# Performance work log

Hardware: AMD Instinct MI355X
Metric: run time of the kernel (lower is better)

The kernel has to match this reference:

```python
import jax, jax.numpy as jnp
import numpy as np

BIAS = (1, 1)


def setup_inputs() -> dict:
    key = jax.random.key(0)
    k1, k2 = jax.random.split(key)
    B, N = 32, 1024
    c = jax.random.normal(k1, (B, 2 * N), dtype=jnp.float32)
    y = jax.random.randint(k2, (B, N), 0, 2, dtype=jnp.int32)
    return {"c": c, "y": y}


def reference(c, y):
    # split_tensor: even columns -> c1 (scores c_{2r}), odd columns -> s1 (thresholds s_{2r+1})
    c1 = c[:, ::2]   # [B, N]
    s1 = c[:, 1::2]  # [B, N]
    yf = y.astype(jnp.float32)
    y_bar = 1.0 - yf

    y_norm = jnp.sum(yf, axis=1) ** BIAS[0]
    y_bar_norm = jnp.sum(y_bar, axis=1) ** BIAS[1]
    denom = 2.0 * y_norm * y_bar_norm + y_norm * y_norm + y_bar_norm * y_bar_norm

    # pairwise_sub_exp(a, b, x) = sum_{k,l} a_k b_l exp(x_l - x_k)
    #                           = (sum_k a_k e^{-x_k}) * (sum_l b_l e^{x_l})  -- fused, no [B,N,N] materialization
    y_exp_neg_c1 = jnp.sum(yf * jnp.exp(-c1), axis=1)      # sum_k y_k e^{-c1_k}
    ybar_exp_c1 = jnp.sum(y_bar * jnp.exp(c1), axis=1)     # sum_l ybar_l e^{c1_l}
    ybar_exp_neg_s1 = jnp.sum(y_bar * jnp.exp(-s1), axis=1)
    y_exp_s1 = jnp.sum(yf * jnp.exp(s1), axis=1)

    p1 = y_exp_neg_c1 * ybar_exp_c1        # pairwise_sub_exp(y, y_bar, c1)
    p2 = ybar_exp_neg_s1 * y_exp_s1        # pairwise_sub_exp(y_bar, y, s1)
    # valueThreshod_sub_exp(a, x, s) = sum_{r,t} a_r a_t exp(s_t - x_r)
    v1 = y_exp_neg_c1 * y_exp_s1           # valueThreshod_sub_exp(y, c1, s1)
    v2 = ybar_exp_neg_s1 * ybar_exp_c1     # valueThreshod_sub_exp(y_bar, s1, c1)

    return jnp.mean((p1 + p2 + v1 + v2) / denom)
```

## Files before the change

### kernel.cpp

```cpp
#include <hip/hip_runtime.h>

#define NCOLS 1024
#define NROWS 32

__global__ __launch_bounds__(256) void bpmll_row_kernel(
    const float* __restrict__ c, const int* __restrict__ y,
    float* __restrict__ ws) {
    const int row = blockIdx.x;
    const int tid = threadIdx.x;
    const float2* __restrict__ crow =
        reinterpret_cast<const float2*>(c + (size_t)row * 2 * NCOLS);
    const int* __restrict__ yrow = y + (size_t)row * NCOLS;

    float sy = 0.f, sA = 0.f, sB = 0.f, sC = 0.f, sD = 0.f;
    #pragma unroll
    for (int k = 0; k < NCOLS / 256; ++k) {
        const int col = k * 256 + tid;
        const float2 cs = crow[col];
        const float yf = (float)yrow[col];
        const float yb = 1.f - yf;
        const float ec  = __expf(cs.x);
        const float enc = __expf(-cs.x);
        const float es  = __expf(cs.y);
        const float ens = __expf(-cs.y);
        sy += yf;
        sA += yf * enc;
        sC += yb * ec;
        sB += yb * ens;
        sD += yf * es;
    }
    #pragma unroll
    for (int off = 32; off > 0; off >>= 1) {
        sy += __shfl_down(sy, off);
        sA += __shfl_down(sA, off);
        sB += __shfl_down(sB, off);
        sC += __shfl_down(sC, off);
        sD += __shfl_down(sD, off);
    }
    __shared__ float red[4][5];
    const int wave = tid >> 6;
    const int lane = tid & 63;
    if (lane == 0) {
        red[wave][0] = sy; red[wave][1] = sA; red[wave][2] = sB;
        red[wave][3] = sC; red[wave][4] = sD;
    }
    __syncthreads();
    if (tid == 0) {
        float ty = 0.f, tA = 0.f, tB = 0.f, tC = 0.f, tD = 0.f;
        #pragma unroll
        for (int w = 0; w < 4; ++w) {
            ty += red[w][0]; tA += red[w][1]; tB += red[w][2];
            tC += red[w][3]; tD += red[w][4];
        }
        const float yn  = ty;
        const float ybn = (float)NCOLS - ty;
        const float denom = 2.f * yn * ybn + yn * yn + ybn * ybn;
        ws[row] = (tA + tB) * (tC + tD) / denom;
    }
}

__global__ __launch_bounds__(64) void bpmll_final_kernel(
    const float* __restrict__ ws, float* __restrict__ out) {
    const int lane = threadIdx.x;
    float v = (lane < NROWS) ? ws[lane] : 0.f;
    #pragma unroll
    for (int off = 32; off > 0; off >>= 1) v += __shfl_down(v, off);
    if (lane == 0) out[0] = v * (1.f / NROWS);
}

extern "C" void kernel_launch(void* const* d_in, const int* in_sizes, int n_in,
                              void* d_out, int out_size, void* d_ws, size_t ws_size,
                              hipStream_t stream) {
    const float* c = (const float*)d_in[0];
    const int*   y = (const int*)d_in[1];
    float* out = (float*)d_out;
    float* ws  = (float*)d_ws;
    bpmll_row_kernel<<<NROWS, 256, 0, stream>>>(c, y, ws);
    bpmll_final_kernel<<<1, 64, 0, stream>>>(ws, out);
}
```

Before: 11.29 us.

## Fuse row and final reductions into one single-block kernel with fewer exps

```diff
diff --git a/kernel.cpp b/kernel.cpp
--- a/kernel.cpp
+++ b/kernel.cpp
@@ -3,69 +3,71 @@
 #define NCOLS 1024
 #define NROWS 32
 
-__global__ __launch_bounds__(256) void bpmll_row_kernel(
+__global__ __launch_bounds__(1024) void bpmll_fused_kernel(
     const float* __restrict__ c, const int* __restrict__ y,
-    float* __restrict__ ws) {
-    const int row = blockIdx.x;
+    float* __restrict__ out) {
     const int tid = threadIdx.x;
-    const float2* __restrict__ crow =
-        reinterpret_cast<const float2*>(c + (size_t)row * 2 * NCOLS);
-    const int* __restrict__ yrow = y + (size_t)row * NCOLS;
-
-    float sy = 0.f, sA = 0.f, sB = 0.f, sC = 0.f, sD = 0.f;
-    #pragma unroll
-    for (int k = 0; k < NCOLS / 256; ++k) {
-        const int col = k * 256 + tid;
-        const float2 cs = crow[col];
-        const float yf = (float)yrow[col];
-        const float yb = 1.f - yf;
-        const float ec  = __expf(cs.x);
-        const float enc = __expf(-cs.x);
-        const float es  = __expf(cs.y);
-        const float ens = __expf(-cs.y);
-        sy += yf;
-        sA += yf * enc;
-        sC += yb * ec;
-        sB += yb * ens;
-        sD += yf * es;
-    }
-    #pragma unroll
-    for (int off = 32; off > 0; off >>= 1) {
-        sy += __shfl_down(sy, off);
-        sA += __shfl_down(sA, off);
-        sB += __shfl_down(sB, off);
-        sC += __shfl_down(sC, off);
-        sD += __shfl_down(sD, off);
-    }
-    __shared__ float red[4][5];
     const int wave = tid >> 6;
     const int lane = tid & 63;
-    if (lane == 0) {
-        red[wave][0] = sy; red[wave][1] = sA; red[wave][2] = sB;
-        red[wave][3] = sC; red[wave][4] = sD;
+    __shared__ float rowv[NROWS];
+
+    #pragma unroll
+    for (int rr = 0; rr < 2; ++rr) {
+        const int row = wave * 2 + rr;
+        const float4* __restrict__ crow4 =
+            reinterpret_cast<const float4*>(c + (size_t)row * 2 * NCOLS);
+        const int2* __restrict__ yrow2 =
+            reinterpret_cast<const int2*>(y + (size_t)row * NCOLS);
+
+        float sy = 0.f, sA = 0.f, sB = 0.f, sC = 0.f, sD = 0.f;
+        #pragma unroll
+        for (int k = 0; k < 8; ++k) {
+            const int idx = k * 64 + lane;
+            const float4 F = crow4[idx];
+            const int2  Y = yrow2[idx];
+            {
+                const bool yy = (Y.x != 0);
+                const float e1 = __expf(yy ? -F.x : F.x);
+                const float e2 = __expf(yy ?  F.y : -F.y);
+                sy += yy ? 1.f : 0.f;
+                sA += yy ? e1 : 0.f;
+                sD += yy ? e2 : 0.f;
+                sC += yy ? 0.f : e1;
+                sB += yy ? 0.f : e2;
+            }
+            {
+                const bool yy = (Y.y != 0);
+                const float e1 = __expf(yy ? -F.z : F.z);
+                const float e2 = __expf(yy ?  F.w : -F.w);
+                sy += yy ? 1.f : 0.f;
+                sA += yy ? e1 : 0.f;
+                sD += yy ? e2 : 0.f;
+                sC += yy ? 0.f : e1;
+                sB += yy ? 0.f : e2;
+            }
+        }
+        #pragma unroll
+        for (int off = 32; off > 0; off >>= 1) {
+            sy += __shfl_xor(sy, off);
+            sA += __shfl_xor(sA, off);
+            sB += __shfl_xor(sB, off);
+            sC += __shfl_xor(sC, off);
+            sD += __shfl_xor(sD, off);
+        }
+        if (lane == 0) {
+            const float yn  = sy;
+            const float ybn = (float)NCOLS - sy;
+            const float denom = 2.f * yn * ybn + yn * yn + ybn * ybn;
+            rowv[row] = (sA + sB) * (sC + sD) / denom;
+        }
     }
     __syncthreads();
-    if (tid == 0) {
-        float ty = 0.f, tA = 0.f, tB = 0.f, tC = 0.f, tD = 0.f;
+    if (tid < 64) {
+        float v = (lane < NROWS) ? rowv[lane] : 0.f;
         #pragma unroll
-        for (int w = 0; w < 4; ++w) {
-            ty += red[w][0]; tA += red[w][1]; tB += red[w][2];
-            tC += red[w][3]; tD += red[w][4];
-        }
-        const float yn  = ty;
-        const float ybn = (float)NCOLS - ty;
-        const float denom = 2.f * yn * ybn + yn * yn + ybn * ybn;
-        ws[row] = (tA + tB) * (tC + tD) / denom;
+        for (int off = 32; off > 0; off >>= 1) v += __shfl_xor(v, off);
+        if (lane == 0) out[0] = v * (1.f / NROWS);
     }
-}
-
-__global__ __launch_bounds__(64) void bpmll_final_kernel(
-    const float* __restrict__ ws, float* __restrict__ out) {
-    const int lane = threadIdx.x;
-    float v = (lane < NROWS) ? ws[lane] : 0.f;
-    #pragma unroll
-    for (int off = 32; off > 0; off >>= 1) v += __shfl_down(v, off);
-    if (lane == 0) out[0] = v * (1.f / NROWS);
 }
 
 extern "C" void kernel_launch(void* const* d_in, const int* in_sizes, int n_in,
@@ -74,7 +76,6 @@
     const float* c = (const float*)d_in[0];
     const int*   y = (const int*)d_in[1];
     float* out = (float*)d_out;
-    float* ws  = (float*)d_ws;
-    bpmll_row_kernel<<<NROWS, 256, 0, stream>>>(c, y, ws);
-    bpmll_final_kernel<<<1, 64, 0, stream>>>(ws, out);
+    (void)d_ws; (void)ws_size;
+    bpmll_fused_kernel<<<1, 1024, 0, stream>>>(c, y, out);
 }
```

After: 11.60 us. 2.8% more time.
